# Kernel tuning notes

Measured on AMD Instinct MI355X. Metric: run time of the kernel, lower is better.

## Reference

```python
import jax, jax.numpy as jnp
import numpy as np
from jax import lax

L, B, N_IN, N_OUT, K = 1024, 16, 1024, 512, 5


def setup_inputs() -> dict:
    key = jax.random.key(0)
    k0, k1, k2, k3, k4 = jax.random.split(key, 5)
    val_range = (6.0 / (N_IN + N_OUT)) ** 0.5
    x = jax.random.normal(k0, (L, B, N_IN), dtype=jnp.float32)
    weight = jax.random.uniform(k1, (N_IN, N_OUT * K), dtype=jnp.float32,
                                minval=-val_range, maxval=val_range)
    bias = jax.random.normal(k2, (N_OUT * K,), dtype=jnp.float32) * 0.1
    bias_eps = jax.random.normal(k3, (N_OUT,), dtype=jnp.float32) * 0.1
    bias_final = jax.random.normal(k4, (N_OUT * 2,), dtype=jnp.float32) * 0.1
    return {"x": x, "weight": weight, "bias": bias,
            "bias_eps": bias_eps, "bias_final": bias_final}


def reference(x, weight, bias, bias_eps, bias_final):
    # x: [L, B, n_in]; unidirectional (bidir=1), real semiring, output gate, tanh
    length, batch, n_in = x.shape
    n_out = N_OUT
    u_ = (x.reshape(-1, n_in) @ weight).reshape(length, batch, n_out, K)
    b = bias.reshape(K, n_out)  # [5, n_out]: in1, in2, f1, f2, out
    forget_bias1, forget_bias2, output_bias = b[2], b[3], b[4]
    output = jax.nn.sigmoid(u_[..., 4] + output_bias)      # [L, B, n_out]
    forget1 = jax.nn.sigmoid(u_[..., 2] + forget_bias1)
    forget2 = jax.nn.sigmoid(u_[..., 3] + forget_bias2)
    u1, u2 = u_[..., 0], u_[..., 1]
    eps = jax.nn.sigmoid(bias_eps)                          # [n_out]

    def step(carry, inp):
        c1_prev, c2_prev = carry
        f1t, f2t, u1t, u2t = inp
        c1_t = c1_prev * f1t + u1t
        c2_t = c2_prev * f2t + (eps + c1_prev) * u2t
        return (c1_t, c2_t), (c1_t, c2_t)

    init = (jnp.zeros((batch, n_out), x.dtype), jnp.zeros((batch, n_out), x.dtype))
    (c1_final, c2_final), (c1s, c2s) = lax.scan(step, init, (forget1, forget2, u1, u2))

    rho = jax.nn.sigmoid(bias_final.reshape(n_out, 2)) * 2.0
    cs = c1s * rho[:, 0] + c2s * rho[:, 1]
    gcs = jnp.tanh(output * cs)                             # [L, B, n_out]
    return gcs, c1_final, c2_final
```

## Files before the change

### kernel.cpp

```cpp
#include <hip/hip_runtime.h>
#include <cstdint>

#define LSEQ 1024
#define BATCH 16
#define NIN 1024
#define NOUT 512
#define KGATE 5
#define NCOL (NOUT * KGATE)
#define MTOT (LSEQ * BATCH)
#define CHAINS (BATCH * NOUT)
#define OUT_GCS (LSEQ * BATCH * NOUT)
#define SEG 32
#define SLEN 32
#define PLANE ((size_t)MTOT * NOUT)
#define SMP ((size_t)SEG * CHAINS)

typedef _Float16 f16x8 __attribute__((ext_vector_type(8)));
typedef _Float16 f16x4 __attribute__((ext_vector_type(4)));
typedef float f32x4 __attribute__((ext_vector_type(4)));

__device__ __forceinline__ void async16(const void* g, void* l) {
    __builtin_amdgcn_global_load_lds(
        (const __attribute__((address_space(1))) void*)(uintptr_t)g,
        (__attribute__((address_space(3))) void*)(uintptr_t)l,
        16, 0, 0);
}

__device__ __forceinline__ float fsigmoid(float x) {
    return 1.0f / (1.0f + __expf(-x));
}

__global__ void convert_x_k(const float* __restrict__ x, _Float16* __restrict__ xb, int n4) {
    int i = blockIdx.x * blockDim.x + threadIdx.x;
    if (i < n4) {
        float4 v = ((const float4*)x)[i];
        f16x4 h;
        h.x = (_Float16)v.x; h.y = (_Float16)v.y; h.z = (_Float16)v.z; h.w = (_Float16)v.w;
        ((f16x4*)xb)[i] = h;
    }
}

__global__ __launch_bounds__(256) void transpose_w_k(const float* __restrict__ w, _Float16* __restrict__ wT) {
    __shared__ float lds[32][33];
    int t = threadIdx.x;
    int col = t & 31;
    int rowg = t >> 5;
    int n0 = blockIdx.x * 32;
    int k0 = blockIdx.y * 32;
#pragma unroll
    for (int i = 0; i < 4; i++) {
        int r = rowg + i * 8;
        lds[r][col] = w[(size_t)(k0 + r) * NCOL + n0 + col];
    }
    __syncthreads();
#pragma unroll
    for (int i = 0; i < 4; i++) {
        int r = rowg + i * 8;
        int c = n0 + r;
        int row = (c % 5) * NOUT + (c / 5);
        wT[(size_t)row * NIN + k0 + col] = (_Float16)lds[col][r];
    }
}

__global__ __launch_bounds__(256) void gemm_gates_k(const _Float16* __restrict__ A,
                                                    const _Float16* __restrict__ BT,
                                                    const float* __restrict__ bias,
                                                    _Float16* __restrict__ planes) {
    __shared__ _Float16 Al[128 * 32];
    __shared__ _Float16 Bl[128 * 32];
    int t = threadIdx.x;
    int w = t >> 6, lane = t & 63;
    int m0 = blockIdx.x * 128, n0 = blockIdx.y * 128;

    f32x4 acc[4][4] = {};

    const int c1 = t, c2 = t + 256;
    const int r1 = c1 >> 2, s1 = c1 & 3;
    const int r2 = c2 >> 2, s2 = c2 & 3;

    const int q = lane >> 4, r16 = lane & 15;
    const int wm = (w >> 1) * 64, wn = (w & 1) * 64;

    for (int kk = 0; kk < NIN; kk += 32) {
        async16(A + (size_t)(m0 + r1) * NIN + kk + s1 * 8, (char*)Al + c1 * 16);
        async16(A + (size_t)(m0 + r2) * NIN + kk + s2 * 8, (char*)Al + c2 * 16);
        async16(BT + (size_t)(n0 + r1) * NIN + kk + s1 * 8, (char*)Bl + c1 * 16);
        async16(BT + (size_t)(n0 + r2) * NIN + kk + s2 * 8, (char*)Bl + c2 * 16);
        __syncthreads();

        f16x8 af[4], bf[4];
#pragma unroll
        for (int i = 0; i < 4; i++)
            af[i] = *(const f16x8*)(Al + (wm + i * 16 + r16) * 32 + q * 8);
#pragma unroll
        for (int j = 0; j < 4; j++)
            bf[j] = *(const f16x8*)(Bl + (wn + j * 16 + r16) * 32 + q * 8);
#pragma unroll
        for (int i = 0; i < 4; i++)
#pragma unroll
            for (int j = 0; j < 4; j++)
                acc[i][j] = __builtin_amdgcn_mfma_f32_16x16x32_f16(af[i], bf[j], acc[i][j], 0, 0, 0);
        __syncthreads();
    }

    int g = n0 >> 9;
    int nb = n0 & (NOUT - 1);
    _Float16* plane = planes + (size_t)g * PLANE;
#pragma unroll
    for (int j = 0; j < 4; j++) {
        int coln = nb + wn + j * 16 + r16;
        float bv = bias[n0 + wn + j * 16 + r16];
#pragma unroll
        for (int i = 0; i < 4; i++) {
#pragma unroll
            for (int reg = 0; reg < 4; reg++) {
                int m = m0 + wm + i * 16 + q * 4 + reg;
                float v = acc[i][j][reg];
                if (g >= 2) v = fsigmoid(v + bv);
                plane[(size_t)m * NOUT + coln] = (_Float16)v;
            }
        }
    }
}

__global__ __launch_bounds__(256) void compose_k(const _Float16* __restrict__ planes,
                                                 const float* __restrict__ beps,
                                                 float* __restrict__ SM) {
    int u = blockIdx.x * 256 + threadIdx.x;
    int t = u & (CHAINS - 1);
    int s = u >> 13;
    int n = t & (NOUT - 1);
    float eps = fsigmoid(beps[n]);
    float a11 = 1.0f, a21 = 0.0f, a22 = 1.0f, b1 = 0.0f, b2 = 0.0f;
#pragma unroll 4
    for (int j = 0; j < SLEN; j++) {
        size_t e = (size_t)(s * SLEN + j) * CHAINS + t;
        float u1 = (float)planes[e];
        float u2 = (float)planes[PLANE + e];
        float f1 = (float)planes[2 * PLANE + e];
        float f2 = (float)planes[3 * PLANE + e];
        float na11 = f1 * a11;
        float na21 = fmaf(u2, a11, f2 * a21);
        float na22 = f2 * a22;
        float nb1  = fmaf(f1, b1, u1);
        float nb2  = fmaf(u2, b1, fmaf(f2, b2, eps * u2));
        a11 = na11; a21 = na21; a22 = na22; b1 = nb1; b2 = nb2;
    }
    size_t idx = (size_t)s * CHAINS + t;
    SM[idx] = a11;
    SM[SMP + idx] = a21;
    SM[2 * SMP + idx] = a22;
    SM[3 * SMP + idx] = b1;
    SM[4 * SMP + idx] = b2;
}

__global__ __launch_bounds__(256) void segscan_k(const float* __restrict__ SM,
                                                 float* __restrict__ segc,
                                                 float* __restrict__ out) {
    int t = blockIdx.x * 256 + threadIdx.x;
    float c1 = 0.0f, c2 = 0.0f;
#pragma unroll
    for (int s = 0; s < SEG; s++) {
        size_t idx = (size_t)s * CHAINS + t;
        segc[idx] = c1;
        segc[SMP + idx] = c2;
        float a11 = SM[idx];
        float a21 = SM[SMP + idx];
        float a22 = SM[2 * SMP + idx];
        float b1  = SM[3 * SMP + idx];
        float b2  = SM[4 * SMP + idx];
        float c1n = fmaf(a11, c1, b1);
        float c2n = fmaf(a21, c1, fmaf(a22, c2, b2));
        c1 = c1n; c2 = c2n;
    }
    out[OUT_GCS + t] = c1;
    out[OUT_GCS + CHAINS + t] = c2;
}

__global__ __launch_bounds__(256) void apply_k(const _Float16* __restrict__ planes,
                                               const float* __restrict__ segc,
                                               const float* __restrict__ beps,
                                               const float* __restrict__ bfin,
                                               float* __restrict__ out) {
    int u = blockIdx.x * 256 + threadIdx.x;
    int t = u & (CHAINS - 1);
    int s = u >> 13;
    int n = t & (NOUT - 1);
    float eps  = fsigmoid(beps[n]);
    float rho0 = 2.0f * fsigmoid(bfin[2 * n]);
    float rho1 = 2.0f * fsigmoid(bfin[2 * n + 1]);
    size_t idx = (size_t)s * CHAINS + t;
    float c1 = segc[idx];
    float c2 = segc[SMP + idx];
#pragma unroll 4
    for (int j = 0; j < SLEN; j++) {
        size_t e = (size_t)(s * SLEN + j) * CHAINS + t;
        float u1 = (float)planes[e];
        float u2 = (float)planes[PLANE + e];
        float f1 = (float)planes[2 * PLANE + e];
        float f2 = (float)planes[3 * PLANE + e];
        float o  = (float)planes[4 * PLANE + e];
        float c1p = c1;
        c1 = fmaf(c1p, f1, u1);
        c2 = fmaf(c2, f2, (eps + c1p) * u2);
        float cs = fmaf(c1, rho0, c2 * rho1);
        float y = o * cs;
        y = fminf(9.0f, fmaxf(-9.0f, y));
        float ex = __expf(2.0f * y);
        out[e] = (ex - 1.0f) / (ex + 1.0f);
    }
}

extern "C" void kernel_launch(void* const* d_in, const int* in_sizes, int n_in,
                              void* d_out, int out_size, void* d_ws, size_t ws_size,
                              hipStream_t stream) {
    const float* x    = (const float*)d_in[0];
    const float* wgt  = (const float*)d_in[1];
    const float* bias = (const float*)d_in[2];
    const float* beps = (const float*)d_in[3];
    const float* bfin = (const float*)d_in[4];
    float* out = (float*)d_out;

    char* p = (char*)d_ws;
    _Float16* wT     = (_Float16*)p; p += (size_t)NCOL * NIN * 2;
    _Float16* xb     = (_Float16*)p; p += (size_t)MTOT * NIN * 2;
    _Float16* planes = (_Float16*)p; p += 5 * PLANE * 2;
    float* SM        = (float*)p;    p += 5 * SMP * 4;
    float* segc      = (float*)p;    p += 2 * SMP * 4;

    transpose_w_k<<<dim3(NCOL / 32, NIN / 32), 256, 0, stream>>>(wgt, wT);

    int n4 = MTOT * NIN / 4;
    convert_x_k<<<dim3((n4 + 255) / 256), 256, 0, stream>>>(x, xb, n4);

    gemm_gates_k<<<dim3(MTOT / 128, NCOL / 128), 256, 0, stream>>>(xb, wT, bias, planes);

    compose_k<<<dim3(CHAINS * SEG / 256), 256, 0, stream>>>(planes, beps, SM);
    segscan_k<<<dim3(CHAINS / 256), 256, 0, stream>>>(SM, segc, out);
    apply_k<<<dim3(CHAINS * SEG / 256), 256, 0, stream>>>(planes, segc, beps, bfin, out);
}
```

Measured before the change: 302.1 us.

## Swizzle GEMM LDS tiles and stage epilogue through LDS for vector stores

XOR-swizzles the 16-byte chunk index used both when async-loading A and B tiles into LDS and when reading MFMA fragments, so fragment reads spread across LDS banks instead of conflicting. The epilogue now writes sigmoid/bias results into a padded LDS tile in two halves and then emits 16-byte vectorized, row-contiguous global stores instead of scattered 2-byte stores. This adds two barriers per half and reuses the tile buffers for staging, with a larger shared allocation.

```diff
diff --git a/kernel.cpp b/kernel.cpp
--- a/kernel.cpp
+++ b/kernel.cpp
@@ -66,8 +66,9 @@
                                                     const _Float16* __restrict__ BT,
                                                     const float* __restrict__ bias,
                                                     _Float16* __restrict__ planes) {
-    __shared__ _Float16 Al[128 * 32];
-    __shared__ _Float16 Bl[128 * 32];
+    __shared__ __align__(16) char smem[17408];
+    _Float16* Al = (_Float16*)smem;
+    _Float16* Bl = (_Float16*)(smem + 8192);
     int t = threadIdx.x;
     int w = t >> 6, lane = t & 63;
     int m0 = blockIdx.x * 128, n0 = blockIdx.y * 128;
@@ -75,11 +76,12 @@
     f32x4 acc[4][4] = {};
 
     const int c1 = t, c2 = t + 256;
-    const int r1 = c1 >> 2, s1 = c1 & 3;
-    const int r2 = c2 >> 2, s2 = c2 & 3;
+    const int r1 = c1 >> 2, s1 = (c1 & 3) ^ (r1 & 3) ^ ((r1 >> 2) & 3);
+    const int r2 = c2 >> 2, s2 = (c2 & 3) ^ (r2 & 3) ^ ((r2 >> 2) & 3);
 
     const int q = lane >> 4, r16 = lane & 15;
     const int wm = (w >> 1) * 64, wn = (w & 1) * 64;
+    const int qs = q ^ (r16 & 3) ^ ((r16 >> 2) & 3);
 
     for (int kk = 0; kk < NIN; kk += 32) {
         async16(A + (size_t)(m0 + r1) * NIN + kk + s1 * 8, (char*)Al + c1 * 16);
@@ -91,10 +93,10 @@
         f16x8 af[4], bf[4];
 #pragma unroll
         for (int i = 0; i < 4; i++)
-            af[i] = *(const f16x8*)(Al + (wm + i * 16 + r16) * 32 + q * 8);
+            af[i] = *(const f16x8*)(Al + (wm + i * 16 + r16) * 32 + qs * 8);
 #pragma unroll
         for (int j = 0; j < 4; j++)
-            bf[j] = *(const f16x8*)(Bl + (wn + j * 16 + r16) * 32 + q * 8);
+            bf[j] = *(const f16x8*)(Bl + (wn + j * 16 + r16) * 32 + qs * 8);
 #pragma unroll
         for (int i = 0; i < 4; i++)
 #pragma unroll
@@ -106,20 +108,38 @@
     int g = n0 >> 9;
     int nb = n0 & (NOUT - 1);
     _Float16* plane = planes + (size_t)g * PLANE;
-#pragma unroll
-    for (int j = 0; j < 4; j++) {
-        int coln = nb + wn + j * 16 + r16;
-        float bv = bias[n0 + wn + j * 16 + r16];
-#pragma unroll
-        for (int i = 0; i < 4; i++) {
-#pragma unroll
-            for (int reg = 0; reg < 4; reg++) {
-                int m = m0 + wm + i * 16 + q * 4 + reg;
-                float v = acc[i][j][reg];
-                if (g >= 2) v = fsigmoid(v + bv);
-                plane[(size_t)m * NOUT + coln] = (_Float16)v;
+    _Float16* T = (_Float16*)smem;
+
+    float bv[4];
+#pragma unroll
+    for (int j = 0; j < 4; j++) bv[j] = bias[n0 + wn + j * 16 + r16];
+
+#pragma unroll
+    for (int h = 0; h < 2; h++) {
+        if ((w >> 1) == h) {
+            int cb = (w & 1) * 64 + r16;
+#pragma unroll
+            for (int j = 0; j < 4; j++) {
+#pragma unroll
+                for (int i = 0; i < 4; i++) {
+#pragma unroll
+                    for (int reg = 0; reg < 4; reg++) {
+                        float v = acc[i][j][reg];
+                        if (g >= 2) v = fsigmoid(v + bv[j]);
+                        T[(i * 16 + q * 4 + reg) * 136 + cb + j * 16] = (_Float16)v;
+                    }
+                }
             }
         }
+        __syncthreads();
+        int seg = t & 15, rr = t >> 4;
+#pragma unroll
+        for (int p = 0; p < 4; p++) {
+            int row = rr + p * 16;
+            f16x8 v = *(const f16x8*)(T + row * 136 + seg * 8);
+            *(f16x8*)(plane + (size_t)(m0 + h * 64 + row) * NOUT + nb + seg * 8) = v;
+        }
+        __syncthreads();
     }
 }
 
```

Result: slower. 313.1 us (+3.7%).
